# Performance work log

Measured on AMD Instinct MI355X. Metric: run time of the kernel, lower is better.

## Reference

```python
import jax, jax.numpy as jnp
import numpy as np

N = 65536          # total nodes
B = 64             # graphs in batch
NPG = N // B       # nodes per graph (equal-size graphs)
K = 128            # n_clusters (assignment dim)
D_IN = 128         # node feature dim
D = 128            # pooled feature dim
E = 1048576        # edges (avg degree 16)


def setup_inputs() -> dict:
    key = jax.random.key(0)
    k1, k2, k3, k4, k5, k6 = jax.random.split(key, 6)
    h = jax.random.normal(k1, (N, D_IN), dtype=jnp.float32)
    fea = jax.random.normal(k2, (B * K, D), dtype=jnp.float32)
    W_self = jax.random.normal(k3, (D_IN, K), dtype=jnp.float32) / np.sqrt(D_IN)
    W_neigh = jax.random.normal(k4, (D_IN, K), dtype=jnp.float32) / np.sqrt(D_IN)
    b = jnp.zeros((K,), dtype=jnp.float32)
    # edges kept within each graph: sample local ids then offset by graph base
    base = jnp.repeat(jnp.arange(B, dtype=jnp.int64) * NPG, E // B)
    edge_src = jax.random.randint(k5, (E,), 0, NPG, dtype=jnp.int64) + base
    edge_dst = jax.random.randint(k6, (E,), 0, NPG, dtype=jnp.int64) + base
    return {"h": h, "fea": fea, "W_self": W_self, "W_neigh": W_neigh,
            "b": b, "edge_src": edge_src, "edge_dst": edge_dst}


def reference(h, fea, W_self, W_neigh, b, edge_src, edge_dst):
    # GraphSage mean aggregation: neigh[i] = mean_{j: (j->i)} h[j]
    deg = jnp.zeros((N,), h.dtype).at[edge_dst].add(1.0)
    neigh = jnp.zeros((N, D_IN), h.dtype).at[edge_dst].add(h[edge_src])
    neigh = neigh / jnp.maximum(deg, 1.0)[:, None]
    assign = jax.nn.relu(h @ W_self + neigh @ W_neigh + b)       # [N, K]
    assign = jax.nn.softmax(assign, axis=1)                       # softmax over clusters
    # block-diagonal mm == per-graph GEMM: [B, n, K] @ [B, K, D] -> [B, n, D]
    out = jnp.einsum('bnk,bkd->bnd',
                     assign.reshape(B, NPG, K),
                     fea.reshape(B, K, D))
    return out.reshape(N, D)
```

## Files before the change

### kernel.cpp

```cpp
#include <hip/hip_runtime.h>

#define N_NODES 65536
#define B_G     64
#define NPG     1024
#define KC      128
#define DIN     128
#define E_EDGES 1048576
#define EPG     16384
#define NSLICE  8
#define SLICE_E (EPG / NSLICE)
#define CSTRIDE (EPG + NPG)

typedef __attribute__((ext_vector_type(8))) short short8;
typedef __attribute__((ext_vector_type(4))) float floatx4;

static __device__ __forceinline__ short f2bf(float x) {
    unsigned u = __float_as_uint(x);
    unsigned r = (u + 0x7FFF + ((u >> 16) & 1)) >> 16;
    return (short)r;
}
static __device__ __forceinline__ unsigned pack2(float a, float b) {
    return (unsigned)(unsigned short)f2bf(a) | ((unsigned)(unsigned short)f2bf(b) << 16);
}

__global__ __launch_bounds__(256) void setup_a(
    const float* __restrict__ Wself, const float* __restrict__ Wneigh,
    const float* __restrict__ fea, const float* __restrict__ h,
    const int* __restrict__ edst,
    short* __restrict__ wt, short* __restrict__ feaT, short* __restrict__ h_bf,
    int* __restrict__ slicecnt)
{
    int bid = blockIdx.x;
    int tid = threadIdx.x;
    if (bid < B_G * NSLICE) {
        __shared__ int cnt[NPG];
        int g = bid >> 3, s = bid & 7;
        int gbase = g << 10;
        for (int i = tid; i < NPG; i += 256) cnt[i] = 0;
        __syncthreads();
        const int* ed = edst + (size_t)g * EPG + s * SLICE_E;
#pragma unroll
        for (int it = 0; it < SLICE_E / 256; it++)
            atomicAdd(&cnt[ed[it * 256 + tid] - gbase], 1);
        __syncthreads();
        int* sc = slicecnt + ((size_t)bid << 10);
        for (int i = tid; i < NPG; i += 256) sc[i] = cnt[i];
    } else {
        long idx = (long)(bid - B_G * NSLICE) * 256 + tid;
        if (idx < 32768) {
            int n = (int)(idx >> 8), k = (int)(idx & 255);
            float v = (k < 128) ? Wself[k * 128 + n] : Wneigh[(k - 128) * 128 + n];
            wt[idx] = f2bf(v);
        } else if (idx < 32768 + 1048576) {
            long fi = idx - 32768;
            int g = (int)(fi >> 14), d = (int)((fi >> 7) & 127), k = (int)(fi & 127);
            feaT[fi] = f2bf(fea[((long)g * 128 + k) * 128 + d]);
        } else {
            long gi = idx - 32768 - 1048576;
            const float4* hp = (const float4*)h + gi * 2;
            float4 a = hp[0], b4 = hp[1];
            uint4 w;
            w.x = pack2(a.x, a.y);
            w.y = pack2(a.z, a.w);
            w.z = pack2(b4.x, b4.y);
            w.w = pack2(b4.z, b4.w);
            ((uint4*)h_bf)[gi] = w;
        }
    }
}

__global__ __launch_bounds__(1024) void setup_b(
    const int* __restrict__ slicecnt, int* __restrict__ offs,
    int* __restrict__ deg, int* __restrict__ sliceoffs)
{
    __shared__ int sa[NPG];
    int g = blockIdx.x;
    int tid = threadIdx.x;
    int s8[NSLICE];
    int d = 0;
#pragma unroll
    for (int s = 0; s < NSLICE; s++) {
        s8[s] = slicecnt[(((size_t)g * NSLICE + s) << 10) + tid];
        d += s8[s];
    }
    int p = (d + 1) & ~1;
    sa[tid] = p;
    __syncthreads();
    for (int off = 1; off < NPG; off <<= 1) {
        int v = sa[tid];
        int vv = (tid >= off) ? sa[tid - off] : 0;
        __syncthreads();
        sa[tid] = v + vv;
        __syncthreads();
    }
    int excl = sa[tid] - p;
    offs[(g << 10) + tid] = excl;
    deg[(g << 10) + tid] = d;
    int run = excl;
#pragma unroll
    for (int s = 0; s < NSLICE; s++) {
        sliceoffs[(((size_t)g * NSLICE + s) << 10) + tid] = run;
        run += s8[s];
    }
}

__global__ __launch_bounds__(256) void setup_c(
    const int* __restrict__ esrc, const int* __restrict__ edst,
    const int* __restrict__ sliceoffs, unsigned short* __restrict__ csr)
{
    __shared__ int cur[NPG];
    int bid = blockIdx.x;
    int tid = threadIdx.x;
    int g = bid >> 3, s = bid & 7;
    int gbase = g << 10;
    const int* so = sliceoffs + ((size_t)bid << 10);
    for (int i = tid; i < NPG; i += 256) cur[i] = so[i];
    __syncthreads();
    const int* ed = edst + (size_t)g * EPG + s * SLICE_E;
    const int* es = esrc + (size_t)g * EPG + s * SLICE_E;
    unsigned short* cg = csr + (size_t)g * CSTRIDE;
#pragma unroll
    for (int it = 0; it < SLICE_E / 256; it++) {
        int e = it * 256 + tid;
        int d = ed[e] - gbase;
        int src = es[e] - gbase;
        int pos = atomicAdd(&cur[d], 1);
        cg[pos] = (unsigned short)src;
    }
}

__global__ __launch_bounds__(256) void agg_kernel(
    const short* __restrict__ h_bf, const unsigned short* __restrict__ csr,
    const int* __restrict__ offs, const int* __restrict__ deg,
    short* __restrict__ neigh)
{
    int g = blockIdx.x >> 8;
    int chunk = blockIdx.x & 255;
    int wave = threadIdx.x >> 6, lane = threadIdx.x & 63;
    int local = chunk * 4 + wave;
    int node = g * NPG + local;
    int start = offs[node];
    int m = deg[node];
    const unsigned short* lst = csr + (size_t)g * CSTRIDE + start;
    const uint2* rows = (const uint2*)h_bf + (size_t)g * NPG * 32;
    int l31 = lane & 31;
    int hi = lane >> 5;
    float s0 = 0.f, s1 = 0.f, s2 = 0.f, s3 = 0.f;
    int pairs = m >> 1;
    int p = 0;
    for (; p + 4 <= pairs; p += 4) {
        unsigned pp[4];
#pragma unroll
        for (int u = 0; u < 4; u++) pp[u] = *(const unsigned*)(lst + 2 * (p + u));
        uint2 v[4];
#pragma unroll
        for (int u = 0; u < 4; u++) {
            int s = hi ? (int)(pp[u] >> 16) : (int)(pp[u] & 0xffff);
            v[u] = rows[s * 32 + l31];
        }
#pragma unroll
        for (int u = 0; u < 4; u++) {
            s0 += __uint_as_float(v[u].x << 16);
            s1 += __uint_as_float(v[u].x & 0xffff0000u);
            s2 += __uint_as_float(v[u].y << 16);
            s3 += __uint_as_float(v[u].y & 0xffff0000u);
        }
    }
    for (; p < pairs; p++) {
        unsigned pp = *(const unsigned*)(lst + 2 * p);
        int s = hi ? (int)(pp >> 16) : (int)(pp & 0xffff);
        uint2 vv = rows[s * 32 + l31];
        s0 += __uint_as_float(vv.x << 16);
        s1 += __uint_as_float(vv.x & 0xffff0000u);
        s2 += __uint_as_float(vv.y << 16);
        s3 += __uint_as_float(vv.y & 0xffff0000u);
    }
    if (m & 1) {
        int s = lst[m - 1];
        if (!hi) {
            uint2 vv = rows[s * 32 + l31];
            s0 += __uint_as_float(vv.x << 16);
            s1 += __uint_as_float(vv.x & 0xffff0000u);
            s2 += __uint_as_float(vv.y << 16);
            s3 += __uint_as_float(vv.y & 0xffff0000u);
        }
    }
    s0 += __shfl_xor(s0, 32, 64);
    s1 += __shfl_xor(s1, 32, 64);
    s2 += __shfl_xor(s2, 32, 64);
    s3 += __shfl_xor(s3, 32, 64);
    if (!hi) {
        float invd = 1.0f / fmaxf((float)m, 1.0f);
        uint2 w;
        w.x = pack2(s0 * invd, s1 * invd);
        w.y = pack2(s2 * invd, s3 * invd);
        ((uint2*)neigh)[(size_t)node * 32 + l31] = w;
    }
}

__global__ __launch_bounds__(256) void fused_kernel(
    const short* __restrict__ h_bf, const short* __restrict__ neigh,
    const short* __restrict__ wt, const float* __restrict__ bias,
    const short* __restrict__ feaT, float* __restrict__ out)
{
    __shared__ __align__(16) short ldsP[64 * 132];

    int tid = threadIdx.x;
    int tile_m = blockIdx.x * 64;
    int g = tile_m >> 10;
    int wave = tid >> 6, lane = tid & 63;
    int l15 = lane & 15, quad = lane >> 4;

    floatx4 zz = {0.f, 0.f, 0.f, 0.f};
    floatx4 acc[8];
#pragma unroll
    for (int j = 0; j < 8; j++) acc[j] = zz;

#pragma unroll
    for (int kk = 0; kk < 4; kk++) {
#pragma unroll
        for (int ks = 0; ks < 2; ks++) {
            int colk = kk * 64 + ks * 32 + quad * 8;
            int m = tile_m + wave * 16 + l15;
            short8 af = (kk < 2)
                ? *reinterpret_cast<const short8*>(h_bf + (size_t)m * DIN + colk)
                : *reinterpret_cast<const short8*>(neigh + (size_t)m * DIN + (colk - 128));
#pragma unroll
            for (int cb = 0; cb < 8; cb++) {
                int n = cb * 16 + l15;
                short8 bf = *reinterpret_cast<const short8*>(wt + n * 256 + colk);
                acc[cb] = __builtin_amdgcn_mfma_f32_16x16x32_bf16(af, bf, acc[cb], 0, 0, 0);
            }
        }
    }

    float bv[8];
#pragma unroll
    for (int cb = 0; cb < 8; cb++) bv[cb] = bias[cb * 16 + l15];

#pragma unroll
    for (int v = 0; v < 4; v++) {
        float x[8];
        float m = -1e30f;
#pragma unroll
        for (int cb = 0; cb < 8; cb++) {
            float t = acc[cb][v] + bv[cb];
            t = fmaxf(t, 0.f);
            x[cb] = t;
            m = fmaxf(m, t);
        }
#pragma unroll
        for (int off = 1; off < 16; off <<= 1) m = fmaxf(m, __shfl_xor(m, off, 64));
        float s = 0.f;
#pragma unroll
        for (int cb = 0; cb < 8; cb++) { x[cb] = __expf(x[cb] - m); s += x[cb]; }
#pragma unroll
        for (int off = 1; off < 16; off <<= 1) s += __shfl_xor(s, off, 64);
        float inv = 1.0f / s;
        int row = wave * 16 + quad * 4 + v;
#pragma unroll
        for (int cb = 0; cb < 8; cb++)
            ldsP[row * 132 + cb * 16 + l15] = f2bf(x[cb] * inv);
    }

    asm volatile("s_waitcnt lgkmcnt(0)" ::: "memory");

    floatx4 oacc[8];
#pragma unroll
    for (int j = 0; j < 8; j++) oacc[j] = zz;

    short8 pf[4];
#pragma unroll
    for (int ks = 0; ks < 4; ks++)
        pf[ks] = *reinterpret_cast<const short8*>(
            ldsP + (wave * 16 + l15) * 132 + ks * 32 + quad * 8);

#pragma unroll
    for (int cb = 0; cb < 8; cb++) {
#pragma unroll
        for (int ks = 0; ks < 4; ks++) {
            short8 bf = *reinterpret_cast<const short8*>(
                feaT + ((size_t)g * 128 + cb * 16 + l15) * 128 + ks * 32 + quad * 8);
            oacc[cb] = __builtin_amdgcn_mfma_f32_16x16x32_bf16(pf[ks], bf, oacc[cb], 0, 0, 0);
        }
    }

#pragma unroll
    for (int v = 0; v < 4; v++) {
        int row = tile_m + wave * 16 + quad * 4 + v;
#pragma unroll
        for (int cb = 0; cb < 8; cb++)
            out[(size_t)row * 128 + cb * 16 + l15] = oacc[cb][v];
    }
}

extern "C" void kernel_launch(void* const* d_in, const int* in_sizes, int n_in,
                              void* d_out, int out_size, void* d_ws, size_t ws_size,
                              hipStream_t stream) {
    const float* h      = (const float*)d_in[0];
    const float* fea    = (const float*)d_in[1];
    const float* Wself  = (const float*)d_in[2];
    const float* Wneigh = (const float*)d_in[3];
    const float* bias   = (const float*)d_in[4];
    const int*   esrc   = (const int*)d_in[5];
    const int*   edst   = (const int*)d_in[6];
    float* out = (float*)d_out;

    char* ws = (char*)d_ws;
    short* h_bf = (short*)ws;
    size_t off = (size_t)N_NODES * DIN * sizeof(short);
    short* neigh = (short*)(ws + off); off += (size_t)N_NODES * DIN * sizeof(short);
    short* wt    = (short*)(ws + off); off += (size_t)128 * 256 * sizeof(short);
    short* feaT  = (short*)(ws + off); off += (size_t)B_G * 128 * 128 * sizeof(short);
    unsigned short* csr = (unsigned short*)(ws + off); off += (size_t)B_G * CSTRIDE * sizeof(short);
    int* offs = (int*)(ws + off); off += (size_t)N_NODES * sizeof(int);
    int* deg  = (int*)(ws + off); off += (size_t)N_NODES * sizeof(int);
    int* slicecnt  = (int*)(ws + off); off += (size_t)B_G * NSLICE * NPG * sizeof(int);
    int* sliceoffs = (int*)(ws + off);

    setup_a<<<B_G * NSLICE + 8320, 256, 0, stream>>>(Wself, Wneigh, fea, h, edst,
                                                     wt, feaT, h_bf, slicecnt);
    setup_b<<<B_G, 1024, 0, stream>>>(slicecnt, offs, deg, sliceoffs);
    setup_c<<<B_G * NSLICE, 256, 0, stream>>>(esrc, edst, sliceoffs, csr);
    agg_kernel<<<256 * B_G, 256, 0, stream>>>(h_bf, csr, offs, deg, neigh);
    fused_kernel<<<N_NODES / 64, 256, 0, stream>>>(h_bf, neigh, wt, bias, feaT, out);
}
```

Measured before the change: 201.3 us.

## Split fused kernel across column waves with register-resident weights and LDS softmax reduction

The fused GEMM+softmax+GEMM kernel now uses 512-thread blocks where each of 8 waves owns a 16-column slice. Each wave keeps its W and fea B-fragments in registers for the whole block and loops over 8 row tiles of 16. This removes the repeated global loads of the weight matrices per row tile. The cost is that the row softmax now needs cross-wave max and sum reductions through LDS with three __syncthreads per tile. A-fragments are also loaded redundantly by all 8 waves, and fewer blocks are launched.

Result: no change. 198.2 us (-1.5%).

```diff
diff --git a/kernel.cpp b/kernel.cpp
--- a/kernel.cpp
+++ b/kernel.cpp
@@ -198,99 +198,118 @@
     }
 }
 
-__global__ __launch_bounds__(256) void fused_kernel(
+__global__ __launch_bounds__(512) void fused_kernel(
     const short* __restrict__ h_bf, const short* __restrict__ neigh,
     const short* __restrict__ wt, const float* __restrict__ bias,
     const short* __restrict__ feaT, float* __restrict__ out)
 {
-    __shared__ __align__(16) short ldsP[64 * 132];
+    __shared__ __align__(16) short ldsP[16 * 132];
+    __shared__ float pmaxLDS[16 * 8];
+    __shared__ float psumLDS[16 * 8];
 
     int tid = threadIdx.x;
-    int tile_m = blockIdx.x * 64;
-    int g = tile_m >> 10;
     int wave = tid >> 6, lane = tid & 63;
     int l15 = lane & 15, quad = lane >> 4;
+    int row0 = blockIdx.x * 128;
+    int g = row0 >> 10;
+    int ncol = wave * 16;
+
+    short8 wtB[8];
+#pragma unroll
+    for (int kk = 0; kk < 8; kk++)
+        wtB[kk] = *reinterpret_cast<const short8*>(
+            wt + (ncol + l15) * 256 + kk * 32 + quad * 8);
+    short8 feaB[4];
+#pragma unroll
+    for (int ks = 0; ks < 4; ks++)
+        feaB[ks] = *reinterpret_cast<const short8*>(
+            feaT + ((size_t)g * 128 + ncol + l15) * 128 + ks * 32 + quad * 8);
+    float bv = bias[ncol + l15];
 
     floatx4 zz = {0.f, 0.f, 0.f, 0.f};
-    floatx4 acc[8];
-#pragma unroll
-    for (int j = 0; j < 8; j++) acc[j] = zz;
-
-#pragma unroll
-    for (int kk = 0; kk < 4; kk++) {
-#pragma unroll
-        for (int ks = 0; ks < 2; ks++) {
-            int colk = kk * 64 + ks * 32 + quad * 8;
-            int m = tile_m + wave * 16 + l15;
-            short8 af = (kk < 2)
-                ? *reinterpret_cast<const short8*>(h_bf + (size_t)m * DIN + colk)
-                : *reinterpret_cast<const short8*>(neigh + (size_t)m * DIN + (colk - 128));
-#pragma unroll
-            for (int cb = 0; cb < 8; cb++) {
-                int n = cb * 16 + l15;
-                short8 bf = *reinterpret_cast<const short8*>(wt + n * 256 + colk);
-                acc[cb] = __builtin_amdgcn_mfma_f32_16x16x32_bf16(af, bf, acc[cb], 0, 0, 0);
-            }
-        }
-    }
-
-    float bv[8];
-#pragma unroll
-    for (int cb = 0; cb < 8; cb++) bv[cb] = bias[cb * 16 + l15];
-
-#pragma unroll
-    for (int v = 0; v < 4; v++) {
-        float x[8];
-        float m = -1e30f;
-#pragma unroll
-        for (int cb = 0; cb < 8; cb++) {
-            float t = acc[cb][v] + bv[cb];
-            t = fmaxf(t, 0.f);
-            x[cb] = t;
-            m = fmaxf(m, t);
-        }
-#pragma unroll
-        for (int off = 1; off < 16; off <<= 1) m = fmaxf(m, __shfl_xor(m, off, 64));
-        float s = 0.f;
-#pragma unroll
-        for (int cb = 0; cb < 8; cb++) { x[cb] = __expf(x[cb] - m); s += x[cb]; }
-#pragma unroll
-        for (int off = 1; off < 16; off <<= 1) s += __shfl_xor(s, off, 64);
-        float inv = 1.0f / s;
-        int row = wave * 16 + quad * 4 + v;
-#pragma unroll
-        for (int cb = 0; cb < 8; cb++)
-            ldsP[row * 132 + cb * 16 + l15] = f2bf(x[cb] * inv);
-    }
-
-    asm volatile("s_waitcnt lgkmcnt(0)" ::: "memory");
-
-    floatx4 oacc[8];
-#pragma unroll
-    for (int j = 0; j < 8; j++) oacc[j] = zz;
-
-    short8 pf[4];
-#pragma unroll
-    for (int ks = 0; ks < 4; ks++)
-        pf[ks] = *reinterpret_cast<const short8*>(
-            ldsP + (wave * 16 + l15) * 132 + ks * 32 + quad * 8);
-
-#pragma unroll
-    for (int cb = 0; cb < 8; cb++) {
-#pragma unroll
-        for (int ks = 0; ks < 4; ks++) {
-            short8 bf = *reinterpret_cast<const short8*>(
-                feaT + ((size_t)g * 128 + cb * 16 + l15) * 128 + ks * 32 + quad * 8);
-            oacc[cb] = __builtin_amdgcn_mfma_f32_16x16x32_bf16(pf[ks], bf, oacc[cb], 0, 0, 0);
-        }
-    }
-
-#pragma unroll
-    for (int v = 0; v < 4; v++) {
-        int row = tile_m + wave * 16 + quad * 4 + v;
-#pragma unroll
-        for (int cb = 0; cb < 8; cb++)
-            out[(size_t)row * 128 + cb * 16 + l15] = oacc[cb][v];
+
+    for (int mt = 0; mt < 8; mt++) {
+        int mrow = row0 + mt * 16;
+
+        short8 af[8];
+#pragma unroll
+        for (int kk = 0; kk < 8; kk++) {
+            const short* ap = (kk < 4)
+                ? h_bf + (size_t)(mrow + l15) * DIN + kk * 32 + quad * 8
+                : neigh + (size_t)(mrow + l15) * DIN + (kk - 4) * 32 + quad * 8;
+            af[kk] = *reinterpret_cast<const short8*>(ap);
+        }
+        floatx4 acc = zz;
+#pragma unroll
+        for (int kk = 0; kk < 8; kk++)
+            acc = __builtin_amdgcn_mfma_f32_16x16x32_bf16(af[kk], wtB[kk], acc, 0, 0, 0);
+
+        float x[4], pm[4];
+#pragma unroll
+        for (int v = 0; v < 4; v++) {
+            float t = fmaxf(acc[v] + bv, 0.f);
+            x[v] = t;
+            pm[v] = t;
+        }
+#pragma unroll
+        for (int off = 1; off < 16; off <<= 1)
+#pragma unroll
+            for (int v = 0; v < 4; v++) pm[v] = fmaxf(pm[v], __shfl_xor(pm[v], off, 64));
+        if (l15 == 0) {
+#pragma unroll
+            for (int v = 0; v < 4; v++) pmaxLDS[(quad * 4 + v) * 8 + wave] = pm[v];
+        }
+        __syncthreads();
+        float gm[4];
+#pragma unroll
+        for (int v = 0; v < 4; v++) {
+            int r = quad * 4 + v;
+            float a = fmaxf(fmaxf(pmaxLDS[r*8+0], pmaxLDS[r*8+1]),
+                            fmaxf(pmaxLDS[r*8+2], pmaxLDS[r*8+3]));
+            float b = fmaxf(fmaxf(pmaxLDS[r*8+4], pmaxLDS[r*8+5]),
+                            fmaxf(pmaxLDS[r*8+6], pmaxLDS[r*8+7]));
+            gm[v] = fmaxf(a, b);
+        }
+        float ps[4];
+#pragma unroll
+        for (int v = 0; v < 4; v++) {
+            x[v] = __expf(x[v] - gm[v]);
+            ps[v] = x[v];
+        }
+#pragma unroll
+        for (int off = 1; off < 16; off <<= 1)
+#pragma unroll
+            for (int v = 0; v < 4; v++) ps[v] += __shfl_xor(ps[v], off, 64);
+        if (l15 == 0) {
+#pragma unroll
+            for (int v = 0; v < 4; v++) psumLDS[(quad * 4 + v) * 8 + wave] = ps[v];
+        }
+        __syncthreads();
+#pragma unroll
+        for (int v = 0; v < 4; v++) {
+            int r = quad * 4 + v;
+            float s = (psumLDS[r*8+0] + psumLDS[r*8+1] + psumLDS[r*8+2] + psumLDS[r*8+3])
+                    + (psumLDS[r*8+4] + psumLDS[r*8+5] + psumLDS[r*8+6] + psumLDS[r*8+7]);
+            float inv = 1.0f / s;
+            ldsP[r * 132 + ncol + l15] = f2bf(x[v] * inv);
+        }
+        __syncthreads();
+
+        short8 pf[4];
+#pragma unroll
+        for (int ks = 0; ks < 4; ks++)
+            pf[ks] = *reinterpret_cast<const short8*>(
+                ldsP + l15 * 132 + ks * 32 + quad * 8);
+        floatx4 oacc = zz;
+#pragma unroll
+        for (int ks = 0; ks < 4; ks++)
+            oacc = __builtin_amdgcn_mfma_f32_16x16x32_bf16(pf[ks], feaB[ks], oacc, 0, 0, 0);
+
+#pragma unroll
+        for (int v = 0; v < 4; v++) {
+            int row = mrow + quad * 4 + v;
+            out[(size_t)row * 128 + ncol + l15] = oacc[v];
+        }
     }
 }
 
@@ -323,5 +342,5 @@
     setup_b<<<B_G, 1024, 0, stream>>>(slicecnt, offs, deg, sliceoffs);
     setup_c<<<B_G * NSLICE, 256, 0, stream>>>(esrc, edst, sliceoffs, csr);
     agg_kernel<<<256 * B_G, 256, 0, stream>>>(h_bf, csr, offs, deg, neigh);
-    fused_kernel<<<N_NODES / 64, 256, 0, stream>>>(h_bf, neigh, wt, bias, feaT, out);
-}
+    fused_kernel<<<N_NODES / 128, 512, 0, stream>>>(h_bf, neigh, wt, bias, feaT, out);
+}
```
